# Kernel optimization log

Hardware: AMD Instinct MI355X
Metric: run time of the kernel (lower is better)

The kernel has to match this reference:

```python
import jax, jax.numpy as jnp
import numpy as np

EMBED_DIM = 1024
TASK_BIAS_DIM = 128
BATCH = 4
SEQ = 2048


def setup_inputs() -> dict:
    key = jax.random.key(0)
    kq, kk, kv, kt, kw, kb = jax.random.split(key, 6)
    query = jax.random.normal(kq, (BATCH, SEQ, EMBED_DIM), dtype=jnp.float32)
    key_t = jax.random.normal(kk, (BATCH, SEQ, EMBED_DIM), dtype=jnp.float32)
    value = jax.random.normal(kv, (BATCH, SEQ, EMBED_DIM), dtype=jnp.float32)
    task_bias = jax.random.normal(kt, (BATCH, TASK_BIAS_DIM), dtype=jnp.float32)
    # task_bias_proj: Linear(task_bias_dim, 1) -> weight [1, task_bias_dim], bias [1]
    lim = 1.0 / np.sqrt(TASK_BIAS_DIM)
    W = jax.random.uniform(kw, (TASK_BIAS_DIM, 1), jnp.float32, -lim, lim)
    b = jax.random.uniform(kb, (1,), jnp.float32, -lim, lim)
    return {"query": query, "key": key_t, "value": value,
            "task_bias": task_bias, "W": W, "b": b}


def reference(query, key, value, task_bias, W, b):
    scale = EMBED_DIM ** 0.5
    # scores: [batch, seq, seq]
    scores = jnp.einsum('bqd,bkd->bqk', query, key) / scale
    # per-batch scalar gate from task bias: [batch, 1]
    gate = jax.nn.sigmoid(task_bias @ W + b)           # [batch, 1]
    scores = scores * gate[:, :, None]                 # broadcast [b,1,1]
    attention_weights = jax.nn.softmax(scores, axis=-1)
    output = jnp.einsum('bqk,bkd->bqd', attention_weights, value)
    return output, attention_weights
```

## Files before the change

kernel.cpp:

```cpp
#include <hip/hip_runtime.h>
#include <hip/hip_bf16.h>
#include <stdint.h>
#include <stddef.h>

#define B_  4
#define S_  2048
#define D_  1024
#define TB_ 128

typedef float v4f  __attribute__((ext_vector_type(4)));
typedef short s16x4 __attribute__((ext_vector_type(4)));
typedef short s16x8 __attribute__((ext_vector_type(8)));

#define WAITV(n) asm volatile("s_waitcnt vmcnt(" #n ")" ::: "memory")

__device__ __forceinline__ unsigned short f2bf(float f) {
  union { float f; unsigned u; } x; x.f = f;
  unsigned u = x.u;
  unsigned r = (u + 0x7FFFu + ((u >> 16) & 1u)) >> 16;
  return (unsigned short)r;
}

__device__ __forceinline__ void gld16(const void* g, void* l) {
  __builtin_amdgcn_global_load_lds(
      (const __attribute__((address_space(1))) unsigned int*)g,
      (__attribute__((address_space(3))) unsigned int*)l, 16, 0, 0);
}

__device__ __forceinline__ void barrier_sync() {
  asm volatile("" ::: "memory");
  __builtin_amdgcn_s_barrier();
  asm volatile("" ::: "memory");
  __builtin_amdgcn_sched_barrier(0);
}

__global__ __launch_bounds__(256) void gate_kernel(
    const float* __restrict__ tb, const float* __restrict__ W,
    const float* __restrict__ bias, float* __restrict__ gate) {
  int t = threadIdx.x;
  int b = t >> 6, l = t & 63;
  float s = tb[b * TB_ + l] * W[l] + tb[b * TB_ + 64 + l] * W[64 + l];
  #pragma unroll
  for (int off = 32; off > 0; off >>= 1) s += __shfl_down(s, off, 64);
  if (l == 0) gate[b] = 1.0f / (1.0f + __expf(-(s + bias[0])));
}

__global__ __launch_bounds__(256) void cvt_bf16_kernel(
    const float* __restrict__ src, short* __restrict__ dst) {
  size_t g = (size_t)blockIdx.x * 256 + threadIdx.x;
  v4f v = *(const v4f*)(src + g * 4);
  s16x4 o;
  o[0] = (short)f2bf(v[0]); o[1] = (short)f2bf(v[1]);
  o[2] = (short)f2bf(v[2]); o[3] = (short)f2bf(v[3]);
  *(s16x4*)(dst + g * 4) = o;
}

__global__ __launch_bounds__(256) void vT_kernel(
    const float* __restrict__ V, short* __restrict__ VT) {
  __shared__ float tile[64][65];
  int b = blockIdx.z;
  int s0 = blockIdx.x * 64, d0 = blockIdx.y * 64;
  int t = threadIdx.x;
  int tc = t & 63, tr4 = t >> 6;
  const float* src = V + ((size_t)b * S_ + s0) * D_ + d0;
  #pragma unroll
  for (int p = 0; p < 16; ++p) {
    int r = p * 4 + tr4;
    tile[r][tc] = src[(size_t)r * D_ + tc];
  }
  __syncthreads();
  short* dst = VT + ((size_t)b * D_ + d0) * S_ + s0;
  #pragma unroll
  for (int p = 0; p < 16; ++p) {
    int r = p * 4 + tr4;
    dst[(size_t)r * S_ + tc] = (short)f2bf(tile[tc][r]);
  }
}

template<int MF, int WNC, int BLOADS, int KT, int BROWS, int LDC, bool GATED>
__global__ __launch_bounds__(512, 2) void gemm_pipe(
    const short* __restrict__ Ag, const short* __restrict__ Bg,
    const float* __restrict__ gate, float* __restrict__ Cg) {
  extern __shared__ char lds[];
  constexpr int NF = 4;
  constexpr int PH = MF / 2;
  constexpr int NT = KT / 64;
  constexpr int BN = WNC * 64;
  constexpr int ABYTES = 256 * 128;
  constexpr int BBYTES = BN * 128;
  constexpr int BUFB = ABYTES + BBYTES;

  int wg = blockIdx.x;
  int swz = (wg & 7) * 32 + (wg >> 3);
  int b = swz >> 6;
  int rem = swz & 63;
  int m0 = (rem >> 3) * 256;
  int n0 = (rem & 7) * BN;

  int tid = threadIdx.x;
  int w = tid >> 6, l = tid & 63;
  int wm = w / WNC, wn = w % WNC;

  const short* Ab = Ag + (size_t)b * S_ * KT + (size_t)m0 * KT;
  const short* Bb = Bg + (size_t)b * BROWS * KT + (size_t)n0 * KT;

  int srow8 = l >> 3;
  int schunk = ((l & 7) ^ srow8) * 8;
  int fr = l & 15;
  int hi = l >> 4;
  int sl0 = ((hi) ^ (l & 7)) * 16;
  int sl1 = ((4 + hi) ^ (l & 7)) * 16;

  v4f acc[MF][NF];
  #pragma unroll
  for (int m = 0; m < MF; ++m)
    #pragma unroll
    for (int n = 0; n < NF; ++n)
      #pragma unroll
      for (int j = 0; j < 4; ++j) acc[m][n][j] = 0.0f;

  auto stage = [&](int t, int buf) {
    char* La = lds + buf * BUFB;
    char* Lb = La + ABYTES;
    const short* As = Ab + (size_t)t * 64 + schunk;
    #pragma unroll
    for (int j = 0; j < 4; ++j) {
      int blk = w * 4 + j;
      gld16(As + (size_t)(blk * 8 + srow8) * KT, La + blk * 1024);
    }
    const short* Bs = Bb + (size_t)t * 64 + schunk;
    #pragma unroll
    for (int j = 0; j < BLOADS; ++j) {
      int blk = w * BLOADS + j;
      gld16(Bs + (size_t)(blk * 8 + srow8) * KT, Lb + blk * 1024);
    }
  };

  stage(0, 0);
  int cur = 0;
  for (int t = 0; t < NT; ++t) {
    if (t + 1 < NT) {
      stage(t + 1, cur ^ 1);
      if constexpr (BLOADS == 4) WAITV(8); else WAITV(6);
    } else {
      WAITV(0);
    }
    barrier_sync();
    const char* base = lds + cur * BUFB;
    const char* Bbase = base + ABYTES;
    s16x8 bfr[NF][2];
    #pragma unroll
    for (int n = 0; n < NF; ++n) {
      const char* rp = Bbase + (size_t)(wn * 64 + n * 16 + fr) * 128;
      bfr[n][0] = *(const s16x8*)(rp + sl0);
      bfr[n][1] = *(const s16x8*)(rp + sl1);
    }
    s16x8 afc[2][2];
    #pragma unroll
    for (int i = 0; i < 2; ++i) {
      const char* rp = base + (size_t)(wm * (MF * 16) + i * 16 + fr) * 128;
      afc[i][0] = *(const s16x8*)(rp + sl0);
      afc[i][1] = *(const s16x8*)(rp + sl1);
    }
    barrier_sync();
    #pragma unroll
    for (int p = 0; p < PH; ++p) {
      s16x8 afn[2][2];
      if (p + 1 < PH) {
        #pragma unroll
        for (int i = 0; i < 2; ++i) {
          const char* rp = base +
              (size_t)(wm * (MF * 16) + (2 * (p + 1) + i) * 16 + fr) * 128;
          afn[i][0] = *(const s16x8*)(rp + sl0);
          afn[i][1] = *(const s16x8*)(rp + sl1);
        }
      }
      __builtin_amdgcn_s_setprio(1);
      #pragma unroll
      for (int kh = 0; kh < 2; ++kh)
        #pragma unroll
        for (int i = 0; i < 2; ++i)
          #pragma unroll
          for (int n = 0; n < NF; ++n)
            acc[2 * p + i][n] = __builtin_amdgcn_mfma_f32_16x16x32_bf16(
                afc[i][kh], bfr[n][kh], acc[2 * p + i][n], 0, 0, 0);
      __builtin_amdgcn_s_setprio(0);
      if (p + 1 < PH) {
        afc[0][0] = afn[0][0]; afc[0][1] = afn[0][1];
        afc[1][0] = afn[1][0]; afc[1][1] = afn[1][1];
      }
      barrier_sync();
    }
    cur ^= 1;
  }

  float g = 1.0f;
  if constexpr (GATED) g = gate[b] * 0.03125f;
  float* Cb = Cg + (size_t)b * S_ * LDC +
              (size_t)(m0 + wm * (MF * 16)) * LDC + n0 + wn * 64;
  #pragma unroll
  for (int mf = 0; mf < MF; ++mf)
    #pragma unroll
    for (int n = 0; n < NF; ++n) {
      int r0 = mf * 16 + hi * 4;
      int c = n * 16 + fr;
      #pragma unroll
      for (int j = 0; j < 4; ++j)
        Cb[(size_t)(r0 + j) * LDC + c] = acc[mf][n][j] * g;
    }
}

__global__ __launch_bounds__(256) void softmax_kernel(
    float* __restrict__ attn, short* __restrict__ attnb) {
  size_t row = blockIdx.x;
  float* p = attn + row * S_;
  int t = threadIdx.x;
  v4f v0 = *(const v4f*)(p + t * 8);
  v4f v1 = *(const v4f*)(p + t * 8 + 4);
  float m = fmaxf(fmaxf(fmaxf(v0[0], v0[1]), fmaxf(v0[2], v0[3])),
                  fmaxf(fmaxf(v1[0], v1[1]), fmaxf(v1[2], v1[3])));
  #pragma unroll
  for (int off = 32; off > 0; off >>= 1) m = fmaxf(m, __shfl_xor(m, off, 64));
  __shared__ float rm[4], rs[4];
  if ((t & 63) == 0) rm[t >> 6] = m;
  __syncthreads();
  m = fmaxf(fmaxf(rm[0], rm[1]), fmaxf(rm[2], rm[3]));
  float e[8]; float sum = 0.0f;
  #pragma unroll
  for (int j = 0; j < 4; ++j) { e[j] = __expf(v0[j] - m); sum += e[j]; }
  #pragma unroll
  for (int j = 0; j < 4; ++j) { e[4 + j] = __expf(v1[j] - m); sum += e[4 + j]; }
  #pragma unroll
  for (int off = 32; off > 0; off >>= 1) sum += __shfl_xor(sum, off, 64);
  if ((t & 63) == 0) rs[t >> 6] = sum;
  __syncthreads();
  sum = rs[0] + rs[1] + rs[2] + rs[3];
  float inv = 1.0f / sum;
  #pragma unroll
  for (int j = 0; j < 4; ++j) v0[j] = e[j] * inv;
  #pragma unroll
  for (int j = 0; j < 4; ++j) v1[j] = e[4 + j] * inv;
  *(v4f*)(p + t * 8) = v0;
  *(v4f*)(p + t * 8 + 4) = v1;
  s16x8 ob;
  ob[0] = (short)f2bf(v0[0]); ob[1] = (short)f2bf(v0[1]);
  ob[2] = (short)f2bf(v0[2]); ob[3] = (short)f2bf(v0[3]);
  ob[4] = (short)f2bf(v1[0]); ob[5] = (short)f2bf(v1[1]);
  ob[6] = (short)f2bf(v1[2]); ob[7] = (short)f2bf(v1[3]);
  *(s16x8*)(attnb + row * S_ + t * 8) = ob;
}

extern "C" void kernel_launch(void* const* d_in, const int* in_sizes, int n_in,
                              void* d_out, int out_size, void* d_ws, size_t ws_size,
                              hipStream_t stream) {
  (void)in_sizes; (void)n_in; (void)out_size; (void)ws_size;
  const float* Q  = (const float*)d_in[0];
  const float* K  = (const float*)d_in[1];
  const float* V  = (const float*)d_in[2];
  const float* tb = (const float*)d_in[3];
  const float* W  = (const float*)d_in[4];
  const float* bias = (const float*)d_in[5];

  float* out  = (float*)d_out;
  float* attn = out + (size_t)B_ * S_ * D_;

  char* ws = (char*)d_ws;
  float* gate = (float*)ws;
  short* Qb = (short*)(ws + 256);
  short* Kb = Qb + (size_t)B_ * S_ * D_;
  short* VT = Kb + (size_t)B_ * S_ * D_;
  short* attnb = Qb;

  auto* qkf = gemm_pipe<8, 4, 4, 1024, 2048, 2048, true>;
  auto* pvf = gemm_pipe<4, 2, 2, 2048, 1024, 1024, false>;
  constexpr int QK_LDS = 2 * (256 + 256) * 64 * 2;
  constexpr int PV_LDS = 2 * (256 + 128) * 64 * 2;
  (void)hipFuncSetAttribute((const void*)qkf,
      hipFuncAttributeMaxDynamicSharedMemorySize, QK_LDS);
  (void)hipFuncSetAttribute((const void*)pvf,
      hipFuncAttributeMaxDynamicSharedMemorySize, PV_LDS);

  gate_kernel<<<1, 256, 0, stream>>>(tb, W, bias, gate);
  cvt_bf16_kernel<<<8192, 256, 0, stream>>>(Q, Qb);
  cvt_bf16_kernel<<<8192, 256, 0, stream>>>(K, Kb);
  vT_kernel<<<dim3(32, 16, 4), 256, 0, stream>>>(V, VT);
  qkf<<<256, 512, QK_LDS, stream>>>(Qb, Kb, gate, attn);
  softmax_kernel<<<8192, 256, 0, stream>>>(attn, attnb);
  pvf<<<256, 512, PV_LDS, stream>>>(attnb, VT, gate, out);
}
```

Baseline: 142.1 us.

## Switch GEMMs to 32x32x16 MFMA and fuse prep kernels into one launch

Replaces the 16x16x32 bf16 MFMA tiling in both GEMMs with 32x32x16 MFMA fragments. This cuts LDS fragment reads per FLOP and simplifies the inner loop, dropping the per-phase A prefetch and per-phase barriers in favour of one barrier per K tile. It also merges the gate, Q/K bf16 conversion and V transpose kernels into a single prep launch to reduce launch overhead. The trade-offs are larger accumulator register pressure, the loss of the A-fragment software pipelining, and a different output-store pattern.

```diff
diff --git a/kernel.cpp b/kernel.cpp
--- a/kernel.cpp
+++ b/kernel.cpp
@@ -9,6 +9,7 @@
 #define TB_ 128
 
 typedef float v4f  __attribute__((ext_vector_type(4)));
+typedef float v16f __attribute__((ext_vector_type(16)));
 typedef short s16x4 __attribute__((ext_vector_type(4)));
 typedef short s16x8 __attribute__((ext_vector_type(8)));
 
@@ -34,58 +35,60 @@
   __builtin_amdgcn_sched_barrier(0);
 }
 
-__global__ __launch_bounds__(256) void gate_kernel(
-    const float* __restrict__ tb, const float* __restrict__ W,
-    const float* __restrict__ bias, float* __restrict__ gate) {
+__global__ __launch_bounds__(256) void prep_kernel(
+    const float* __restrict__ Q, const float* __restrict__ K,
+    const float* __restrict__ V, const float* __restrict__ tb,
+    const float* __restrict__ W, const float* __restrict__ bias,
+    short* __restrict__ Qb, short* __restrict__ Kb,
+    short* __restrict__ VT, float* __restrict__ gate) {
+  __shared__ float tile[64][65];
+  int bid = blockIdx.x;
   int t = threadIdx.x;
-  int b = t >> 6, l = t & 63;
-  float s = tb[b * TB_ + l] * W[l] + tb[b * TB_ + 64 + l] * W[64 + l];
-  #pragma unroll
-  for (int off = 32; off > 0; off >>= 1) s += __shfl_down(s, off, 64);
-  if (l == 0) gate[b] = 1.0f / (1.0f + __expf(-(s + bias[0])));
-}
-
-__global__ __launch_bounds__(256) void cvt_bf16_kernel(
-    const float* __restrict__ src, short* __restrict__ dst) {
-  size_t g = (size_t)blockIdx.x * 256 + threadIdx.x;
-  v4f v = *(const v4f*)(src + g * 4);
-  s16x4 o;
-  o[0] = (short)f2bf(v[0]); o[1] = (short)f2bf(v[1]);
-  o[2] = (short)f2bf(v[2]); o[3] = (short)f2bf(v[3]);
-  *(s16x4*)(dst + g * 4) = o;
-}
-
-__global__ __launch_bounds__(256) void vT_kernel(
-    const float* __restrict__ V, short* __restrict__ VT) {
-  __shared__ float tile[64][65];
-  int b = blockIdx.z;
-  int s0 = blockIdx.x * 64, d0 = blockIdx.y * 64;
-  int t = threadIdx.x;
-  int tc = t & 63, tr4 = t >> 6;
-  const float* src = V + ((size_t)b * S_ + s0) * D_ + d0;
-  #pragma unroll
-  for (int p = 0; p < 16; ++p) {
-    int r = p * 4 + tr4;
-    tile[r][tc] = src[(size_t)r * D_ + tc];
+  if (bid < 16384) {
+    const float* src = bid < 8192 ? Q : K;
+    short* dst = bid < 8192 ? Qb : Kb;
+    size_t g = (size_t)(bid & 8191) * 256 + t;
+    v4f v = *(const v4f*)(src + g * 4);
+    s16x4 o;
+    o[0] = (short)f2bf(v[0]); o[1] = (short)f2bf(v[1]);
+    o[2] = (short)f2bf(v[2]); o[3] = (short)f2bf(v[3]);
+    *(s16x4*)(dst + g * 4) = o;
+  } else if (bid < 18432) {
+    int v = bid - 16384;
+    int b = v >> 9;
+    int rem = v & 511;
+    int s0 = (rem & 31) * 64, d0 = (rem >> 5) * 64;
+    int tc = t & 63, tr4 = t >> 6;
+    const float* src = V + ((size_t)b * S_ + s0) * D_ + d0;
+    #pragma unroll
+    for (int p = 0; p < 16; ++p) {
+      int r = p * 4 + tr4;
+      tile[r][tc] = src[(size_t)r * D_ + tc];
+    }
+    __syncthreads();
+    short* dst = VT + ((size_t)b * D_ + d0) * S_ + s0;
+    #pragma unroll
+    for (int p = 0; p < 16; ++p) {
+      int r = p * 4 + tr4;
+      dst[(size_t)r * S_ + tc] = (short)f2bf(tile[tc][r]);
+    }
+  } else {
+    int b = t >> 6, l = t & 63;
+    float s = tb[b * TB_ + l] * W[l] + tb[b * TB_ + 64 + l] * W[64 + l];
+    #pragma unroll
+    for (int off = 32; off > 0; off >>= 1) s += __shfl_down(s, off, 64);
+    if (l == 0) gate[b] = 1.0f / (1.0f + __expf(-(s + bias[0])));
   }
-  __syncthreads();
-  short* dst = VT + ((size_t)b * D_ + d0) * S_ + s0;
-  #pragma unroll
-  for (int p = 0; p < 16; ++p) {
-    int r = p * 4 + tr4;
-    dst[(size_t)r * S_ + tc] = (short)f2bf(tile[tc][r]);
-  }
-}
-
-template<int MF, int WNC, int BLOADS, int KT, int BROWS, int LDC, bool GATED>
+}
+
+template<int MFR, int NFR, int WNC, int BLOADS, int KT, int BROWS, int LDC,
+         bool GATED>
 __global__ __launch_bounds__(512, 2) void gemm_pipe(
     const short* __restrict__ Ag, const short* __restrict__ Bg,
     const float* __restrict__ gate, float* __restrict__ Cg) {
   extern __shared__ char lds[];
-  constexpr int NF = 4;
-  constexpr int PH = MF / 2;
   constexpr int NT = KT / 64;
-  constexpr int BN = WNC * 64;
+  constexpr int BN = WNC * NFR * 32;
   constexpr int ABYTES = 256 * 128;
   constexpr int BBYTES = BN * 128;
   constexpr int BUFB = ABYTES + BBYTES;
@@ -100,24 +103,21 @@
   int tid = threadIdx.x;
   int w = tid >> 6, l = tid & 63;
   int wm = w / WNC, wn = w % WNC;
+  int l7 = l & 7, col31 = l & 31, hi2 = l >> 5;
 
   const short* Ab = Ag + (size_t)b * S_ * KT + (size_t)m0 * KT;
   const short* Bb = Bg + (size_t)b * BROWS * KT + (size_t)n0 * KT;
 
   int srow8 = l >> 3;
   int schunk = ((l & 7) ^ srow8) * 8;
-  int fr = l & 15;
-  int hi = l >> 4;
-  int sl0 = ((hi) ^ (l & 7)) * 16;
-  int sl1 = ((4 + hi) ^ (l & 7)) * 16;
-
-  v4f acc[MF][NF];
-  #pragma unroll
-  for (int m = 0; m < MF; ++m)
-    #pragma unroll
-    for (int n = 0; n < NF; ++n)
-      #pragma unroll
-      for (int j = 0; j < 4; ++j) acc[m][n][j] = 0.0f;
+
+  v16f acc[MFR][NFR];
+  #pragma unroll
+  for (int m = 0; m < MFR; ++m)
+    #pragma unroll
+    for (int n = 0; n < NFR; ++n)
+      #pragma unroll
+      for (int j = 0; j < 16; ++j) acc[m][n][j] = 0.0f;
 
   auto stage = [&](int t, int buf) {
     char* La = lds + buf * BUFB;
@@ -146,67 +146,49 @@
       WAITV(0);
     }
     barrier_sync();
-    const char* base = lds + cur * BUFB;
-    const char* Bbase = base + ABYTES;
-    s16x8 bfr[NF][2];
-    #pragma unroll
-    for (int n = 0; n < NF; ++n) {
-      const char* rp = Bbase + (size_t)(wn * 64 + n * 16 + fr) * 128;
-      bfr[n][0] = *(const s16x8*)(rp + sl0);
-      bfr[n][1] = *(const s16x8*)(rp + sl1);
-    }
-    s16x8 afc[2][2];
-    #pragma unroll
-    for (int i = 0; i < 2; ++i) {
-      const char* rp = base + (size_t)(wm * (MF * 16) + i * 16 + fr) * 128;
-      afc[i][0] = *(const s16x8*)(rp + sl0);
-      afc[i][1] = *(const s16x8*)(rp + sl1);
+    const char* Abase = lds + cur * BUFB;
+    const char* Bbase = Abase + ABYTES;
+    #pragma unroll
+    for (int ks = 0; ks < 4; ++ks) {
+      int slot = ((ks * 2 + hi2) ^ l7) * 16;
+      s16x8 bfr[NFR], af[MFR];
+      #pragma unroll
+      for (int n = 0; n < NFR; ++n)
+        bfr[n] = *(const s16x8*)(Bbase +
+                 (size_t)(wn * (NFR * 32) + n * 32 + col31) * 128 + slot);
+      #pragma unroll
+      for (int m = 0; m < MFR; ++m)
+        af[m] = *(const s16x8*)(Abase +
+                 (size_t)(wm * (MFR * 32) + m * 32 + col31) * 128 + slot);
+      __builtin_amdgcn_s_setprio(1);
+      #pragma unroll
+      for (int m = 0; m < MFR; ++m)
+        #pragma unroll
+        for (int n = 0; n < NFR; ++n)
+          acc[m][n] = __builtin_amdgcn_mfma_f32_32x32x16_bf16(
+              af[m], bfr[n], acc[m][n], 0, 0, 0);
+      __builtin_amdgcn_s_setprio(0);
     }
     barrier_sync();
-    #pragma unroll
-    for (int p = 0; p < PH; ++p) {
-      s16x8 afn[2][2];
-      if (p + 1 < PH) {
-        #pragma unroll
-        for (int i = 0; i < 2; ++i) {
-          const char* rp = base +
-              (size_t)(wm * (MF * 16) + (2 * (p + 1) + i) * 16 + fr) * 128;
-          afn[i][0] = *(const s16x8*)(rp + sl0);
-          afn[i][1] = *(const s16x8*)(rp + sl1);
-        }
-      }
-      __builtin_amdgcn_s_setprio(1);
-      #pragma unroll
-      for (int kh = 0; kh < 2; ++kh)
-        #pragma unroll
-        for (int i = 0; i < 2; ++i)
-          #pragma unroll
-          for (int n = 0; n < NF; ++n)
-            acc[2 * p + i][n] = __builtin_amdgcn_mfma_f32_16x16x32_bf16(
-                afc[i][kh], bfr[n][kh], acc[2 * p + i][n], 0, 0, 0);
-      __builtin_amdgcn_s_setprio(0);
-      if (p + 1 < PH) {
-        afc[0][0] = afn[0][0]; afc[0][1] = afn[0][1];
-        afc[1][0] = afn[1][0]; afc[1][1] = afn[1][1];
-      }
-      barrier_sync();
-    }
     cur ^= 1;
   }
 
   float g = 1.0f;
   if constexpr (GATED) g = gate[b] * 0.03125f;
   float* Cb = Cg + (size_t)b * S_ * LDC +
-              (size_t)(m0 + wm * (MF * 16)) * LDC + n0 + wn * 64;
-  #pragma unroll
-  for (int mf = 0; mf < MF; ++mf)
-    #pragma unroll
-    for (int n = 0; n < NF; ++n) {
-      int r0 = mf * 16 + hi * 4;
-      int c = n * 16 + fr;
-      #pragma unroll
-      for (int j = 0; j < 4; ++j)
-        Cb[(size_t)(r0 + j) * LDC + c] = acc[mf][n][j] * g;
+              (size_t)(m0 + wm * (MFR * 32)) * LDC + n0 + wn * (NFR * 32);
+  #pragma unroll
+  for (int mf = 0; mf < MFR; ++mf)
+    #pragma unroll
+    for (int nf = 0; nf < NFR; ++nf) {
+      int c = nf * 32 + col31;
+      #pragma unroll
+      for (int q = 0; q < 4; ++q)
+        #pragma unroll
+        for (int j = 0; j < 4; ++j) {
+          int r = mf * 32 + q * 8 + 4 * hi2 + j;
+          Cb[(size_t)r * LDC + c] = acc[mf][nf][q * 4 + j] * g;
+        }
     }
 }
 
@@ -271,8 +253,8 @@
   short* VT = Kb + (size_t)B_ * S_ * D_;
   short* attnb = Qb;
 
-  auto* qkf = gemm_pipe<8, 4, 4, 1024, 2048, 2048, true>;
-  auto* pvf = gemm_pipe<4, 2, 2, 2048, 1024, 1024, false>;
+  auto* qkf = gemm_pipe<4, 2, 4, 4, 1024, 2048, 2048, true>;
+  auto* pvf = gemm_pipe<2, 2, 2, 2, 2048, 1024, 1024, false>;
   constexpr int QK_LDS = 2 * (256 + 256) * 64 * 2;
   constexpr int PV_LDS = 2 * (256 + 128) * 64 * 2;
   (void)hipFuncSetAttribute((const void*)qkf,
@@ -280,10 +262,8 @@
   (void)hipFuncSetAttribute((const void*)pvf,
       hipFuncAttributeMaxDynamicSharedMemorySize, PV_LDS);
 
-  gate_kernel<<<1, 256, 0, stream>>>(tb, W, bias, gate);
-  cvt_bf16_kernel<<<8192, 256, 0, stream>>>(Q, Qb);
-  cvt_bf16_kernel<<<8192, 256, 0, stream>>>(K, Kb);
-  vT_kernel<<<dim3(32, 16, 4), 256, 0, stream>>>(V, VT);
+  prep_kernel<<<18433, 256, 0, stream>>>(Q, K, V, tb, W, bias,
+                                         Qb, Kb, VT, gate);
   qkf<<<256, 512, QK_LDS, stream>>>(Qb, Kb, gate, attn);
   softmax_kernel<<<8192, 256, 0, stream>>>(attn, attnb);
   pvf<<<256, 512, PV_LDS, stream>>>(attnb, VT, gate, out);
```

After: 136.9 us. -3.6%, faster.
